# Performance work log

Hardware: AMD Instinct MI355X
Metric: run time of the kernel (lower is better)

The kernel has to match this reference:

```python
import jax, jax.numpy as jnp
import numpy as np

N = 50000      # nodes
F_IN = 512     # input features
HID = 128      # hidden
CLS = 64       # classes
E = 800000     # edges (avg degree 16)
EPS = 1e-5


def setup_inputs() -> dict:
    key = jax.random.key(0)
    k = jax.random.split(key, 6)
    x = jax.random.normal(k[0], (N, F_IN), jnp.float32)
    edge_index = jax.random.randint(k[1], (2, E), 0, N, dtype=jnp.int32)
    W1 = jax.random.normal(k[2], (F_IN, HID), jnp.float32) / np.float32(np.sqrt(F_IN))
    b1 = jnp.zeros((HID,), jnp.float32)
    W2 = jax.random.normal(k[3], (HID, CLS), jnp.float32) / np.float32(np.sqrt(HID))
    b2 = jnp.zeros((CLS,), jnp.float32)
    return {"x": x, "edge_index": edge_index, "W1": W1, "b1": b1, "W2": W2, "b2": b2}


def bin_active(x):
    # BinActive(scalar=True): per-node sign binarization scaled by mean |x| over features
    return jnp.sign(x) * jnp.mean(jnp.abs(x), axis=1, keepdims=True)


def bin_weight(w):
    # binarized weight with per-output-channel scaling (XNOR-style)
    return jnp.sign(w) * jnp.mean(jnp.abs(w), axis=0, keepdims=True)


def gcn_norm(edge_index, n):
    # add self-loops, symmetric D^-1/2 (A+I) D^-1/2 normalization (cached in original)
    loops = jnp.arange(n, dtype=edge_index.dtype)
    row = jnp.concatenate([edge_index[0], loops])  # source
    col = jnp.concatenate([edge_index[1], loops])  # target
    deg = jax.ops.segment_sum(jnp.ones(row.shape[0], jnp.float32), col, num_segments=n)
    dinv = jnp.where(deg > 0, jax.lax.rsqrt(jnp.maximum(deg, 1.0)), 0.0)
    return row, col, dinv[row] * dinv[col]


def bigcn_conv(x, W, b, row, col, norm, n):
    h = x @ bin_weight(W)                                   # [n, out]
    msg = norm[:, None] * h[row]                            # gather + scale, [E+n, out]
    return jax.ops.segment_sum(msg, col, num_segments=n) + b


def reference(x, edge_index, W1, b1, W2, b2):
    n = x.shape[0]
    # BatchNorm1d(affine=False), batch statistics (biased var)
    mu = jnp.mean(x, axis=0)
    var = jnp.var(x, axis=0)
    x = (x - mu) * jax.lax.rsqrt(var + EPS)
    row, col, norm = gcn_norm(edge_index, n)
    # layer loop: BinActive -> (dropout is identity in eval) -> BiGCNConv
    x = bigcn_conv(bin_active(x), W1, b1, row, col, norm, n)
    x = bigcn_conv(bin_active(x), W2, b2, row, col, norm, n)
    return jax.nn.log_softmax(x, axis=1)
```

## Files before the change

### kernel.cpp

```cpp
#include <hip/hip_runtime.h>

typedef unsigned long long u64;

#define F_IN 512
#define HID 128
#define CLS 64
#define EPS 1e-5f
#define NSB 512

__global__ __launch_bounds__(256) void col_stats_k(const float4* __restrict__ x4,
                                                   float* __restrict__ psum,
                                                   float* __restrict__ psq,
                                                   int n, int rpb) {
    __shared__ float red[256][9];
    int c4 = threadIdx.x & 127;
    int half = threadIdx.x >> 7;
    int r0 = blockIdx.x * rpb;
    int r1 = min(n, r0 + rpb);
    float s0=0.f,s1=0.f,s2=0.f,s3=0.f,q0=0.f,q1=0.f,q2=0.f,q3=0.f;
#pragma unroll 4
    for (int r = r0 + half; r < r1; r += 2) {
        float4 v = x4[(size_t)r * 128 + c4];
        s0 += v.x; q0 += v.x * v.x;
        s1 += v.y; q1 += v.y * v.y;
        s2 += v.z; q2 += v.z * v.z;
        s3 += v.w; q3 += v.w * v.w;
    }
    red[threadIdx.x][0]=s0; red[threadIdx.x][1]=s1; red[threadIdx.x][2]=s2; red[threadIdx.x][3]=s3;
    red[threadIdx.x][4]=q0; red[threadIdx.x][5]=q1; red[threadIdx.x][6]=q2; red[threadIdx.x][7]=q3;
    __syncthreads();
    if (half == 0) {
        int c = c4 * 4;
        float* os = &psum[(size_t)blockIdx.x * 512 + c];
        float* oq = &psq [(size_t)blockIdx.x * 512 + c];
        os[0] = s0 + red[c4+128][0]; os[1] = s1 + red[c4+128][1];
        os[2] = s2 + red[c4+128][2]; os[3] = s3 + red[c4+128][3];
        oq[0] = q0 + red[c4+128][4]; oq[1] = q1 + red[c4+128][5];
        oq[2] = q2 + red[c4+128][6]; oq[3] = q3 + red[c4+128][7];
    }
}

__global__ __launch_bounds__(256) void stats_reduce_k(const float* __restrict__ psum,
                                                      const float* __restrict__ psq,
                                                      float* __restrict__ mu,
                                                      float* __restrict__ rinv, int n) {
    __shared__ float reds[256], redq[256];
    int cc = threadIdx.x & 31;
    int bs = threadIdx.x >> 5;
    int c = blockIdx.x * 32 + cc;
    float s = 0.f, q = 0.f;
#pragma unroll 4
    for (int b = bs; b < NSB; b += 8) {
        s += psum[(size_t)b * 512 + c];
        q += psq [(size_t)b * 512 + c];
    }
    reds[threadIdx.x] = s; redq[threadIdx.x] = q;
    __syncthreads();
    if (bs == 0) {
#pragma unroll
        for (int t = 1; t < 8; ++t) { s += reds[cc + 32*t]; q += redq[cc + 32*t]; }
        float m = s / (float)n;
        float v = q / (float)n - m * m;
        mu[c] = m;
        rinv[c] = rsqrtf(v + EPS);
    }
}

__global__ __launch_bounds__(64) void pack_w1_k(const float* __restrict__ W,
                                                u64* __restrict__ sig,
                                                float* __restrict__ beta) {
    int j = blockIdx.x;
    int l = threadIdx.x;
    float asum = 0.f;
#pragma unroll
    for (int jw = 0; jw < 8; ++jw) {
        int f = (jw < 4) ? (4*l + jw) : (256 + 4*l + (jw - 4));
        float v = W[(size_t)f * HID + j];
        asum += fabsf(v);
        u64 b = __ballot(v > 0.0f);
        if (l == 0) sig[jw * HID + j] = b;
    }
    for (int m = 32; m >= 1; m >>= 1) asum += __shfl_xor(asum, m);
    if (l == 0) beta[j] = asum * (1.0f / 512.0f);
}

__global__ __launch_bounds__(64) void pack_w2_k(const float* __restrict__ W,
                                                float* __restrict__ sw4) {
    int j = blockIdx.x;
    int l = threadIdx.x;
    float v0 = W[(size_t)l * CLS + j];
    float v1 = W[(size_t)(l + 64) * CLS + j];
    float asum = fabsf(v0) + fabsf(v1);
    for (int m = 32; m >= 1; m >>= 1) asum += __shfl_xor(asum, m);
    float beta = asum * (1.0f / 128.0f);
    int f0 = l, f1 = l + 64;
    sw4[(f0 >> 2) * 256 + j * 4 + (f0 & 3)] = (v0 > 0.f) ? beta : -beta;
    sw4[(f1 >> 2) * 256 + j * 4 + (f1 & 3)] = (v1 > 0.f) ? beta : -beta;
}

__global__ __launch_bounds__(256) void deg_k(const int* __restrict__ col,
                                             int* __restrict__ deg, int e) {
    int i = blockIdx.x * blockDim.x + threadIdx.x;
    if (i < e) atomicAdd(&deg[col[i]], 1);
}

__global__ __launch_bounds__(256) void dinv_k(const int* __restrict__ deg,
                                              float* __restrict__ dinv, int n) {
    int i = blockIdx.x * blockDim.x + threadIdx.x;
    if (i < n) dinv[i] = rsqrtf((float)deg[i] + 1.0f);
}

__global__ __launch_bounds__(256) void scan_partial_k(const int* __restrict__ deg,
                                                      int* __restrict__ bsum, int n) {
    __shared__ int lds[256];
    int i = blockIdx.x * 256 + threadIdx.x;
    lds[threadIdx.x] = (i < n) ? deg[i] : 0;
    __syncthreads();
    for (int s = 128; s > 0; s >>= 1) {
        if (threadIdx.x < s) lds[threadIdx.x] += lds[threadIdx.x + s];
        __syncthreads();
    }
    if (threadIdx.x == 0) bsum[blockIdx.x] = lds[0];
}

__global__ __launch_bounds__(256) void scan_bsum_k(const int* __restrict__ bsum,
                                                   int* __restrict__ boff, int nb) {
    __shared__ int lds[256];
    int t = threadIdx.x;
    int v = (t < nb) ? bsum[t] : 0;
    lds[t] = v;
    __syncthreads();
    for (int s = 1; s < 256; s <<= 1) {
        int add = (t >= s) ? lds[t - s] : 0;
        __syncthreads();
        lds[t] += add;
        __syncthreads();
    }
    if (t < nb) boff[t] = lds[t] - v;
}

__global__ __launch_bounds__(256) void scan_final_k(const int* __restrict__ deg,
                                                    const int* __restrict__ boff,
                                                    int* __restrict__ offs,
                                                    int* __restrict__ cursor, int n) {
    __shared__ int lds[256];
    int t = threadIdx.x;
    int i = blockIdx.x * 256 + t;
    int v = (i < n) ? deg[i] : 0;
    lds[t] = v;
    __syncthreads();
    for (int s = 1; s < 256; s <<= 1) {
        int add = (t >= s) ? lds[t - s] : 0;
        __syncthreads();
        lds[t] += add;
        __syncthreads();
    }
    int excl = lds[t] - v + boff[blockIdx.x];
    if (i < n) { offs[i] = excl; cursor[i] = excl; }
}

__global__ __launch_bounds__(256) void fill_k(const int* __restrict__ row,
                                              const int* __restrict__ col,
                                              const float* __restrict__ dinv,
                                              int* __restrict__ cursor,
                                              int2* __restrict__ csr, int e) {
    int i = blockIdx.x * blockDim.x + threadIdx.x;
    if (i < e) {
        int r = row[i], c = col[i];
        int p = atomicAdd(&cursor[c], 1);
        float w = dinv[r] * dinv[c];
        csr[p] = make_int2(r, __float_as_int(w));
    }
}

__global__ __launch_bounds__(256) void bin1_gemm1_k(const float4* __restrict__ x4,
                                                    const float4* __restrict__ mu4,
                                                    const float4* __restrict__ rinv4,
                                                    const u64* __restrict__ sigW,
                                                    float* __restrict__ a1,
                                                    short2* __restrict__ dots, int n) {
    int tid = threadIdx.x;
    int wave = tid >> 6, l = tid & 63;
    int i = blockIdx.x * 4 + wave;
    if (i >= n) return;
    const float4* xr = x4 + (size_t)i * 128;
    float4 va = xr[l], vb = xr[64 + l];
    float4 ma = mu4[l], mb = mu4[64 + l];
    float4 ra = rinv4[l], rb = rinv4[64 + l];
    float t0 = va.x - ma.x, t1 = va.y - ma.y, t2 = va.z - ma.z, t3 = va.w - ma.w;
    float t4 = vb.x - mb.x, t5 = vb.y - mb.y, t6 = vb.z - mb.z, t7 = vb.w - mb.w;
    float asum = fabsf(t0)*ra.x + fabsf(t1)*ra.y + fabsf(t2)*ra.z + fabsf(t3)*ra.w
               + fabsf(t4)*rb.x + fabsf(t5)*rb.y + fabsf(t6)*rb.z + fabsf(t7)*rb.w;
    u64 sx[8];
    sx[0] = __ballot(t0 > 0.f); sx[1] = __ballot(t1 > 0.f);
    sx[2] = __ballot(t2 > 0.f); sx[3] = __ballot(t3 > 0.f);
    sx[4] = __ballot(t4 > 0.f); sx[5] = __ballot(t5 > 0.f);
    sx[6] = __ballot(t6 > 0.f); sx[7] = __ballot(t7 > 0.f);
    for (int m = 32; m >= 1; m >>= 1) asum += __shfl_xor(asum, m);
    if (l == 0) a1[i] = asum * (1.0f / 512.0f);
    int c0 = 0, c1 = 0;
#pragma unroll
    for (int w = 0; w < 8; ++w) {
        c0 += __popcll(sx[w] ^ sigW[w * HID + 2*l]);
        c1 += __popcll(sx[w] ^ sigW[w * HID + 2*l + 1]);
    }
    dots[(size_t)i * 64 + l] = make_short2((short)(512 - 2*c0), (short)(512 - 2*c1));
}

__global__ __launch_bounds__(256) void agg1_fused_k(const short2* __restrict__ dots,
                                                    const float* __restrict__ a1,
                                                    const int2* __restrict__ csr,
                                                    const int* __restrict__ offs,
                                                    const int* __restrict__ deg,
                                                    const float* __restrict__ dinv,
                                                    const float2* __restrict__ beta1_2,
                                                    const float2* __restrict__ b1_2,
                                                    u64* __restrict__ sig2x,
                                                    float* __restrict__ a2v, int n) {
    int tid = threadIdx.x;
    int wave = tid >> 6, l = tid & 63;
    int i = blockIdx.x * 4 + wave;
    if (i >= n) return;
    float di = dinv[i];
    float ts = di * di * a1[i];
    short2 ds = dots[(size_t)i * 64 + l];
    float acc0 = ts * (float)ds.x;
    float acc1 = ts * (float)ds.y;
    int off = offs[i], d = deg[i];
    int k = 0;
    for (; k + 4 <= d; k += 4) {
        int2 e0 = csr[off+k], e1 = csr[off+k+1], e2 = csr[off+k+2], e3 = csr[off+k+3];
        float t0 = __int_as_float(e0.y) * a1[e0.x];
        float t1 = __int_as_float(e1.y) * a1[e1.x];
        float t2 = __int_as_float(e2.y) * a1[e2.x];
        float t3 = __int_as_float(e3.y) * a1[e3.x];
        short2 d0 = dots[(size_t)e0.x * 64 + l];
        short2 d1 = dots[(size_t)e1.x * 64 + l];
        short2 d2 = dots[(size_t)e2.x * 64 + l];
        short2 d3 = dots[(size_t)e3.x * 64 + l];
        acc0 += t0*(float)d0.x + t1*(float)d1.x + t2*(float)d2.x + t3*(float)d3.x;
        acc1 += t0*(float)d0.y + t1*(float)d1.y + t2*(float)d2.y + t3*(float)d3.y;
    }
    for (; k < d; ++k) {
        int2 ew = csr[off + k];
        float t = __int_as_float(ew.y) * a1[ew.x];
        short2 dv = dots[(size_t)ew.x * 64 + l];
        acc0 += t * (float)dv.x;
        acc1 += t * (float)dv.y;
    }
    float2 be = beta1_2[l], bb = b1_2[l];
    acc0 = be.x * acc0 + bb.x;
    acc1 = be.y * acc1 + bb.y;
    float asum = fabsf(acc0) + fabsf(acc1);
    for (int m = 32; m >= 1; m >>= 1) asum += __shfl_xor(asum, m);
    u64 s0 = __ballot(acc0 > 0.f);
    u64 s1 = __ballot(acc1 > 0.f);
    if (l == 0) {
        sig2x[2 * (size_t)i]     = s0;
        sig2x[2 * (size_t)i + 1] = s1;
        a2v[i] = asum * (1.0f / 128.0f);
    }
}

__global__ __launch_bounds__(256) void aggz2_fused_k(const u64* __restrict__ sig2x,
                                                     const float* __restrict__ a2v,
                                                     const int2* __restrict__ csr,
                                                     const int* __restrict__ offs,
                                                     const int* __restrict__ deg,
                                                     const float* __restrict__ dinv,
                                                     const float* __restrict__ sw4,
                                                     const float* __restrict__ b2,
                                                     float* __restrict__ out, int n) {
    __shared__ float sw[CLS * HID];
    __shared__ float4 zbuf[4][32];
    int tid = threadIdx.x;
    for (int idx = tid; idx < CLS * HID; idx += 256) sw[idx] = sw4[idx];
    __syncthreads();
    int wave = tid >> 6, l = tid & 63;
    float bias = b2[l];
    for (int q = 0; q < 4; ++q) {
        int i = blockIdx.x * 16 + wave * 4 + q;
        if (i >= n) continue;
        float di = dinv[i];
        float ts = di * di * a2v[i];
        ulonglong2 ws = *(const ulonglong2*)&sig2x[2 * (size_t)i];
        float z0 = ((ws.x >> l) & 1) ? ts : -ts;
        float z1 = ((ws.y >> l) & 1) ? ts : -ts;
        int off = offs[i], d = deg[i];
        int k = 0;
        for (; k + 4 <= d; k += 4) {
            int2 e0 = csr[off+k], e1 = csr[off+k+1], e2 = csr[off+k+2], e3 = csr[off+k+3];
            ulonglong2 g0 = *(const ulonglong2*)&sig2x[2 * (size_t)e0.x];
            ulonglong2 g1 = *(const ulonglong2*)&sig2x[2 * (size_t)e1.x];
            ulonglong2 g2 = *(const ulonglong2*)&sig2x[2 * (size_t)e2.x];
            ulonglong2 g3 = *(const ulonglong2*)&sig2x[2 * (size_t)e3.x];
            float t0 = __int_as_float(e0.y) * a2v[e0.x];
            float t1 = __int_as_float(e1.y) * a2v[e1.x];
            float t2 = __int_as_float(e2.y) * a2v[e2.x];
            float t3 = __int_as_float(e3.y) * a2v[e3.x];
            z0 += (((g0.x>>l)&1) ? t0 : -t0) + (((g1.x>>l)&1) ? t1 : -t1)
                + (((g2.x>>l)&1) ? t2 : -t2) + (((g3.x>>l)&1) ? t3 : -t3);
            z1 += (((g0.y>>l)&1) ? t0 : -t0) + (((g1.y>>l)&1) ? t1 : -t1)
                + (((g2.y>>l)&1) ? t2 : -t2) + (((g3.y>>l)&1) ? t3 : -t3);
        }
        for (; k < d; ++k) {
            int2 ew = csr[off + k];
            ulonglong2 gs = *(const ulonglong2*)&sig2x[2 * (size_t)ew.x];
            float t = __int_as_float(ew.y) * a2v[ew.x];
            z0 += ((gs.x >> l) & 1) ? t : -t;
            z1 += ((gs.y >> l) & 1) ? t : -t;
        }
        ((float2*)&zbuf[wave][0])[l] = make_float2(z0, z1);
        float o = bias;
#pragma unroll
        for (int g = 0; g < 32; ++g) {
            float4 zz = zbuf[wave][g];
            float4 ww = *(const float4*)&sw[g * 256 + l * 4];
            o += zz.x*ww.x + zz.y*ww.y + zz.z*ww.z + zz.w*ww.w;
        }
        float m = o;
        for (int k2 = 32; k2 >= 1; k2 >>= 1) m = fmaxf(m, __shfl_xor(m, k2));
        float ev = __expf(o - m);
        float s = ev;
        for (int k2 = 32; k2 >= 1; k2 >>= 1) s += __shfl_xor(s, k2);
        out[(size_t)i * CLS + l] = o - m - __logf(s);
    }
}

extern "C" void kernel_launch(void* const* d_in, const int* in_sizes, int n_in,
                              void* d_out, int out_size, void* d_ws, size_t ws_size,
                              hipStream_t stream) {
    const float* x  = (const float*)d_in[0];
    const int*   ei = (const int*)d_in[1];
    const float* W1 = (const float*)d_in[2];
    const float* b1 = (const float*)d_in[3];
    const float* W2 = (const float*)d_in[4];
    const float* b2 = (const float*)d_in[5];
    float* out = (float*)d_out;

    const int n = in_sizes[0] / F_IN;
    const int e = in_sizes[1] / 2;
    const int* row = ei;
    const int* col = ei + e;

    char* w = (char*)d_ws;
    size_t off = 0;
    auto alloc = [&](size_t bytes) {
        void* p = w + off;
        off += (bytes + 255) & ~(size_t)255;
        return p;
    };
    int*   deg    = (int*)alloc((size_t)n * 4);
    size_t zero_bytes = off;
    float* psum   = (float*)alloc((size_t)NSB * 512 * 4);
    float* psq    = (float*)alloc((size_t)NSB * 512 * 4);
    float* mu     = (float*)alloc(F_IN * 4);
    float* rinv   = (float*)alloc(F_IN * 4);
    float* dinv   = (float*)alloc((size_t)n * 4);
    float* beta1  = (float*)alloc(HID * 4);
    u64*   sig1   = (u64*)alloc(HID * 8 * 8);
    float* sw4    = (float*)alloc(CLS * HID * 4);
    int*   offs   = (int*)alloc((size_t)n * 4);
    int*   cursor = (int*)alloc((size_t)n * 4);
    int*   bsum   = (int*)alloc(256 * 4);
    int*   boff   = (int*)alloc(256 * 4);
    int2*  csr    = (int2*)alloc((size_t)e * 8);
    short2* dots  = (short2*)alloc((size_t)n * 64 * 4);
    float* a1     = (float*)alloc((size_t)n * 4);
    u64*   sig2x  = (u64*)alloc((size_t)n * 2 * 8);
    float* a2v    = (float*)alloc((size_t)n * 4);
    (void)ws_size;

    hipMemsetAsync(d_ws, 0, zero_bytes, stream);

    int rpb = (n + NSB - 1) / NSB;
    col_stats_k<<<NSB, 256, 0, stream>>>((const float4*)x, psum, psq, n, rpb);
    stats_reduce_k<<<16, 256, 0, stream>>>(psum, psq, mu, rinv, n);
    pack_w1_k<<<HID, 64, 0, stream>>>(W1, sig1, beta1);
    pack_w2_k<<<CLS, 64, 0, stream>>>(W2, sw4);
    deg_k<<<(e + 255) / 256, 256, 0, stream>>>(col, deg, e);
    dinv_k<<<(n + 255) / 256, 256, 0, stream>>>(deg, dinv, n);

    int nb = (n + 255) / 256;
    scan_partial_k<<<nb, 256, 0, stream>>>(deg, bsum, n);
    scan_bsum_k<<<1, 256, 0, stream>>>(bsum, boff, nb);
    scan_final_k<<<nb, 256, 0, stream>>>(deg, boff, offs, cursor, n);
    fill_k<<<(e + 255) / 256, 256, 0, stream>>>(row, col, dinv, cursor, csr, e);

    bin1_gemm1_k<<<(n + 3) / 4, 256, 0, stream>>>((const float4*)x, (const float4*)mu,
                                                  (const float4*)rinv, sig1, a1, dots, n);
    agg1_fused_k<<<(n + 3) / 4, 256, 0, stream>>>(dots, a1, csr, offs, deg, dinv,
                                                  (const float2*)beta1, (const float2*)b1,
                                                  sig2x, a2v, n);
    aggz2_fused_k<<<(n + 15) / 16, 256, 0, stream>>>(sig2x, a2v, csr, offs, deg, dinv,
                                                     sw4, b2, out, n);
}
```

Before: 415.7 us.

## Pre-bake per-source scale factors into CSR edge weights for both aggregation layers

Fuses the dinv computation into the scan kernel and moves CSR fill after the first binarized GEMM, so each layer-1 edge weight already includes the source node's a1 scale. A second CSR copy is rescaled by a2v in a new rebake kernel before layer 2, which removes a random per-edge scale gather from both aggregation loops. Layer-2 aggregation now processes 16 nodes per wave instead of 4, amortizing the shared-memory load of W2, and that load plus the sig2x store are vectorized. In exchange it writes and reads an extra edge array and adds a full pass over the edges.

Result: slower. 435.1 us (+4.7%).

```diff
diff --git a/kernel.cpp b/kernel.cpp
--- a/kernel.cpp
+++ b/kernel.cpp
@@ -104,12 +104,6 @@
     if (i < e) atomicAdd(&deg[col[i]], 1);
 }
 
-__global__ __launch_bounds__(256) void dinv_k(const int* __restrict__ deg,
-                                              float* __restrict__ dinv, int n) {
-    int i = blockIdx.x * blockDim.x + threadIdx.x;
-    if (i < n) dinv[i] = rsqrtf((float)deg[i] + 1.0f);
-}
-
 __global__ __launch_bounds__(256) void scan_partial_k(const int* __restrict__ deg,
                                                       int* __restrict__ bsum, int n) {
     __shared__ int lds[256];
@@ -142,7 +136,8 @@
 __global__ __launch_bounds__(256) void scan_final_k(const int* __restrict__ deg,
                                                     const int* __restrict__ boff,
                                                     int* __restrict__ offs,
-                                                    int* __restrict__ cursor, int n) {
+                                                    int* __restrict__ cursor,
+                                                    float* __restrict__ dinv, int n) {
     __shared__ int lds[256];
     int t = threadIdx.x;
     int i = blockIdx.x * 256 + t;
@@ -156,20 +151,9 @@
         __syncthreads();
     }
     int excl = lds[t] - v + boff[blockIdx.x];
-    if (i < n) { offs[i] = excl; cursor[i] = excl; }
-}
-
-__global__ __launch_bounds__(256) void fill_k(const int* __restrict__ row,
-                                              const int* __restrict__ col,
-                                              const float* __restrict__ dinv,
-                                              int* __restrict__ cursor,
-                                              int2* __restrict__ csr, int e) {
-    int i = blockIdx.x * blockDim.x + threadIdx.x;
-    if (i < e) {
-        int r = row[i], c = col[i];
-        int p = atomicAdd(&cursor[c], 1);
-        float w = dinv[r] * dinv[c];
-        csr[p] = make_int2(r, __float_as_int(w));
+    if (i < n) {
+        offs[i] = excl; cursor[i] = excl;
+        dinv[i] = rsqrtf((float)v + 1.0f);
     }
 }
 
@@ -207,9 +191,26 @@
     dots[(size_t)i * 64 + l] = make_short2((short)(512 - 2*c0), (short)(512 - 2*c1));
 }
 
+__global__ __launch_bounds__(256) void fill_k(const int* __restrict__ row,
+                                              const int* __restrict__ col,
+                                              const float* __restrict__ dinv,
+                                              const float* __restrict__ a1,
+                                              int* __restrict__ cursor,
+                                              int2* __restrict__ csr1,
+                                              int2* __restrict__ csrw, int e) {
+    int i = blockIdx.x * blockDim.x + threadIdx.x;
+    if (i < e) {
+        int r = row[i], c = col[i];
+        int p = atomicAdd(&cursor[c], 1);
+        float w = dinv[r] * dinv[c];
+        csr1[p] = make_int2(r, __float_as_int(w * a1[r]));
+        csrw[p] = make_int2(r, __float_as_int(w));
+    }
+}
+
 __global__ __launch_bounds__(256) void agg1_fused_k(const short2* __restrict__ dots,
                                                     const float* __restrict__ a1,
-                                                    const int2* __restrict__ csr,
+                                                    const int2* __restrict__ csr1,
                                                     const int* __restrict__ offs,
                                                     const int* __restrict__ deg,
                                                     const float* __restrict__ dinv,
@@ -229,11 +230,11 @@
     int off = offs[i], d = deg[i];
     int k = 0;
     for (; k + 4 <= d; k += 4) {
-        int2 e0 = csr[off+k], e1 = csr[off+k+1], e2 = csr[off+k+2], e3 = csr[off+k+3];
-        float t0 = __int_as_float(e0.y) * a1[e0.x];
-        float t1 = __int_as_float(e1.y) * a1[e1.x];
-        float t2 = __int_as_float(e2.y) * a1[e2.x];
-        float t3 = __int_as_float(e3.y) * a1[e3.x];
+        int2 e0 = csr1[off+k], e1 = csr1[off+k+1], e2 = csr1[off+k+2], e3 = csr1[off+k+3];
+        float t0 = __int_as_float(e0.y);
+        float t1 = __int_as_float(e1.y);
+        float t2 = __int_as_float(e2.y);
+        float t3 = __int_as_float(e3.y);
         short2 d0 = dots[(size_t)e0.x * 64 + l];
         short2 d1 = dots[(size_t)e1.x * 64 + l];
         short2 d2 = dots[(size_t)e2.x * 64 + l];
@@ -242,8 +243,8 @@
         acc1 += t0*(float)d0.y + t1*(float)d1.y + t2*(float)d2.y + t3*(float)d3.y;
     }
     for (; k < d; ++k) {
-        int2 ew = csr[off + k];
-        float t = __int_as_float(ew.y) * a1[ew.x];
+        int2 ew = csr1[off + k];
+        float t = __int_as_float(ew.y);
         short2 dv = dots[(size_t)ew.x * 64 + l];
         acc0 += t * (float)dv.x;
         acc1 += t * (float)dv.y;
@@ -256,30 +257,40 @@
     u64 s0 = __ballot(acc0 > 0.f);
     u64 s1 = __ballot(acc1 > 0.f);
     if (l == 0) {
-        sig2x[2 * (size_t)i]     = s0;
-        sig2x[2 * (size_t)i + 1] = s1;
+        ulonglong2 pk; pk.x = s0; pk.y = s1;
+        *(ulonglong2*)&sig2x[2 * (size_t)i] = pk;
         a2v[i] = asum * (1.0f / 128.0f);
+    }
+}
+
+__global__ __launch_bounds__(256) void rebake_k(int2* __restrict__ csrw,
+                                                const float* __restrict__ a2v, int e) {
+    int i = blockIdx.x * blockDim.x + threadIdx.x;
+    if (i < e) {
+        int2 ew = csrw[i];
+        csrw[i] = make_int2(ew.x, __float_as_int(__int_as_float(ew.y) * a2v[ew.x]));
     }
 }
 
 __global__ __launch_bounds__(256) void aggz2_fused_k(const u64* __restrict__ sig2x,
                                                      const float* __restrict__ a2v,
-                                                     const int2* __restrict__ csr,
+                                                     const int2* __restrict__ csrw,
                                                      const int* __restrict__ offs,
                                                      const int* __restrict__ deg,
                                                      const float* __restrict__ dinv,
-                                                     const float* __restrict__ sw4,
+                                                     const float4* __restrict__ sw4,
                                                      const float* __restrict__ b2,
                                                      float* __restrict__ out, int n) {
     __shared__ float sw[CLS * HID];
-    __shared__ float4 zbuf[4][32];
+    __shared__ float zbuf[4][HID];
     int tid = threadIdx.x;
-    for (int idx = tid; idx < CLS * HID; idx += 256) sw[idx] = sw4[idx];
+    for (int idx = tid; idx < CLS * HID / 4; idx += 256)
+        *(float4*)&sw[idx * 4] = sw4[idx];
     __syncthreads();
     int wave = tid >> 6, l = tid & 63;
     float bias = b2[l];
-    for (int q = 0; q < 4; ++q) {
-        int i = blockIdx.x * 16 + wave * 4 + q;
+    for (int q = 0; q < 16; ++q) {
+        int i = blockIdx.x * 64 + wave * 16 + q;
         if (i >= n) continue;
         float di = dinv[i];
         float ts = di * di * a2v[i];
@@ -289,24 +300,24 @@
         int off = offs[i], d = deg[i];
         int k = 0;
         for (; k + 4 <= d; k += 4) {
-            int2 e0 = csr[off+k], e1 = csr[off+k+1], e2 = csr[off+k+2], e3 = csr[off+k+3];
+            int2 e0 = csrw[off+k], e1 = csrw[off+k+1], e2 = csrw[off+k+2], e3 = csrw[off+k+3];
             ulonglong2 g0 = *(const ulonglong2*)&sig2x[2 * (size_t)e0.x];
             ulonglong2 g1 = *(const ulonglong2*)&sig2x[2 * (size_t)e1.x];
             ulonglong2 g2 = *(const ulonglong2*)&sig2x[2 * (size_t)e2.x];
             ulonglong2 g3 = *(const ulonglong2*)&sig2x[2 * (size_t)e3.x];
-            float t0 = __int_as_float(e0.y) * a2v[e0.x];
-            float t1 = __int_as_float(e1.y) * a2v[e1.x];
-            float t2 = __int_as_float(e2.y) * a2v[e2.x];
-            float t3 = __int_as_float(e3.y) * a2v[e3.x];
+            float t0 = __int_as_float(e0.y);
+            float t1 = __int_as_float(e1.y);
+            float t2 = __int_as_float(e2.y);
+            float t3 = __int_as_float(e3.y);
             z0 += (((g0.x>>l)&1) ? t0 : -t0) + (((g1.x>>l)&1) ? t1 : -t1)
                 + (((g2.x>>l)&1) ? t2 : -t2) + (((g3.x>>l)&1) ? t3 : -t3);
             z1 += (((g0.y>>l)&1) ? t0 : -t0) + (((g1.y>>l)&1) ? t1 : -t1)
                 + (((g2.y>>l)&1) ? t2 : -t2) + (((g3.y>>l)&1) ? t3 : -t3);
         }
         for (; k < d; ++k) {
-            int2 ew = csr[off + k];
+            int2 ew = csrw[off + k];
             ulonglong2 gs = *(const ulonglong2*)&sig2x[2 * (size_t)ew.x];
-            float t = __int_as_float(ew.y) * a2v[ew.x];
+            float t = __int_as_float(ew.y);
             z0 += ((gs.x >> l) & 1) ? t : -t;
             z1 += ((gs.y >> l) & 1) ? t : -t;
         }
@@ -314,7 +325,7 @@
         float o = bias;
 #pragma unroll
         for (int g = 0; g < 32; ++g) {
-            float4 zz = zbuf[wave][g];
+            float4 zz = *(const float4*)&zbuf[wave][g * 4];
             float4 ww = *(const float4*)&sw[g * 256 + l * 4];
             o += zz.x*ww.x + zz.y*ww.y + zz.z*ww.z + zz.w*ww.w;
         }
@@ -364,7 +375,8 @@
     int*   cursor = (int*)alloc((size_t)n * 4);
     int*   bsum   = (int*)alloc(256 * 4);
     int*   boff   = (int*)alloc(256 * 4);
-    int2*  csr    = (int2*)alloc((size_t)e * 8);
+    int2*  csr1   = (int2*)alloc((size_t)e * 8);
+    int2*  csrw   = (int2*)alloc((size_t)e * 8);
     short2* dots  = (short2*)alloc((size_t)n * 64 * 4);
     float* a1     = (float*)alloc((size_t)n * 4);
     u64*   sig2x  = (u64*)alloc((size_t)n * 2 * 8);
@@ -379,19 +391,19 @@
     pack_w1_k<<<HID, 64, 0, stream>>>(W1, sig1, beta1);
     pack_w2_k<<<CLS, 64, 0, stream>>>(W2, sw4);
     deg_k<<<(e + 255) / 256, 256, 0, stream>>>(col, deg, e);
-    dinv_k<<<(n + 255) / 256, 256, 0, stream>>>(deg, dinv, n);
 
     int nb = (n + 255) / 256;
     scan_partial_k<<<nb, 256, 0, stream>>>(deg, bsum, n);
     scan_bsum_k<<<1, 256, 0, stream>>>(bsum, boff, nb);
-    scan_final_k<<<nb, 256, 0, stream>>>(deg, boff, offs, cursor, n);
-    fill_k<<<(e + 255) / 256, 256, 0, stream>>>(row, col, dinv, cursor, csr, e);
+    scan_final_k<<<nb, 256, 0, stream>>>(deg, boff, offs, cursor, dinv, n);
 
     bin1_gemm1_k<<<(n + 3) / 4, 256, 0, stream>>>((const float4*)x, (const float4*)mu,
                                                   (const float4*)rinv, sig1, a1, dots, n);
-    agg1_fused_k<<<(n + 3) / 4, 256, 0, stream>>>(dots, a1, csr, offs, deg, dinv,
+    fill_k<<<(e + 255) / 256, 256, 0, stream>>>(row, col, dinv, a1, cursor, csr1, csrw, e);
+    agg1_fused_k<<<(n + 3) / 4, 256, 0, stream>>>(dots, a1, csr1, offs, deg, dinv,
                                                   (const float2*)beta1, (const float2*)b1,
                                                   sig2x, a2v, n);
-    aggz2_fused_k<<<(n + 15) / 16, 256, 0, stream>>>(sig2x, a2v, csr, offs, deg, dinv,
-                                                     sw4, b2, out, n);
-}
+    rebake_k<<<(e + 255) / 256, 256, 0, stream>>>(csrw, a2v, e);
+    aggz2_fused_k<<<(n + 63) / 64, 256, 0, stream>>>(sig2x, a2v, csrw, offs, deg, dinv,
+                                                     (const float4*)sw4, b2, out, n);
+}
```

## Replace layer-2 aggregation and matmul with XNOR-popcount over binarized signatures

Applied to the files above, without the earlier changes.

Layer 2 is now computed per output class as the popcount of the XOR between each neighbour's 128-bit sign signature and the packed weight sign bits, scaled by the edge weight and the per-node scale. This removes the LDS-staged 128x64 float matmul and the per-lane z accumulation that came before it, and it exploits the fact that both operands are ±1 times a scale. The dinv computation is folded into scan_final, which drops one launch, and fill_k is moved after the layer-1 GEMM. The cost is that every lane now gathers the full signature for each edge, and the order of summation changes slightly.

Measured after the change: 384.9 us. -7.4%, faster.

```diff
diff --git a/kernel.cpp b/kernel.cpp
--- a/kernel.cpp
+++ b/kernel.cpp
@@ -85,29 +85,27 @@
 }
 
 __global__ __launch_bounds__(64) void pack_w2_k(const float* __restrict__ W,
-                                                float* __restrict__ sw4) {
+                                                ulonglong2* __restrict__ sigw2,
+                                                float* __restrict__ beta2) {
     int j = blockIdx.x;
     int l = threadIdx.x;
-    float v0 = W[(size_t)l * CLS + j];
-    float v1 = W[(size_t)(l + 64) * CLS + j];
+    float v0 = W[(size_t)(2 * l) * CLS + j];
+    float v1 = W[(size_t)(2 * l + 1) * CLS + j];
     float asum = fabsf(v0) + fabsf(v1);
+    u64 s0 = __ballot(v0 > 0.0f);
+    u64 s1 = __ballot(v1 > 0.0f);
     for (int m = 32; m >= 1; m >>= 1) asum += __shfl_xor(asum, m);
-    float beta = asum * (1.0f / 128.0f);
-    int f0 = l, f1 = l + 64;
-    sw4[(f0 >> 2) * 256 + j * 4 + (f0 & 3)] = (v0 > 0.f) ? beta : -beta;
-    sw4[(f1 >> 2) * 256 + j * 4 + (f1 & 3)] = (v1 > 0.f) ? beta : -beta;
+    if (l == 0) {
+        ulonglong2 t; t.x = s0; t.y = s1;
+        sigw2[j] = t;
+        beta2[j] = asum * (1.0f / 128.0f);
+    }
 }
 
 __global__ __launch_bounds__(256) void deg_k(const int* __restrict__ col,
                                              int* __restrict__ deg, int e) {
     int i = blockIdx.x * blockDim.x + threadIdx.x;
     if (i < e) atomicAdd(&deg[col[i]], 1);
-}
-
-__global__ __launch_bounds__(256) void dinv_k(const int* __restrict__ deg,
-                                              float* __restrict__ dinv, int n) {
-    int i = blockIdx.x * blockDim.x + threadIdx.x;
-    if (i < n) dinv[i] = rsqrtf((float)deg[i] + 1.0f);
 }
 
 __global__ __launch_bounds__(256) void scan_partial_k(const int* __restrict__ deg,
@@ -142,7 +140,8 @@
 __global__ __launch_bounds__(256) void scan_final_k(const int* __restrict__ deg,
                                                     const int* __restrict__ boff,
                                                     int* __restrict__ offs,
-                                                    int* __restrict__ cursor, int n) {
+                                                    int* __restrict__ cursor,
+                                                    float* __restrict__ dinv, int n) {
     __shared__ int lds[256];
     int t = threadIdx.x;
     int i = blockIdx.x * 256 + t;
@@ -156,7 +155,10 @@
         __syncthreads();
     }
     int excl = lds[t] - v + boff[blockIdx.x];
-    if (i < n) { offs[i] = excl; cursor[i] = excl; }
+    if (i < n) {
+        offs[i] = excl; cursor[i] = excl;
+        dinv[i] = rsqrtf((float)v + 1.0f);
+    }
 }
 
 __global__ __launch_bounds__(256) void fill_k(const int* __restrict__ row,
@@ -256,75 +258,66 @@
     u64 s0 = __ballot(acc0 > 0.f);
     u64 s1 = __ballot(acc1 > 0.f);
     if (l == 0) {
-        sig2x[2 * (size_t)i]     = s0;
-        sig2x[2 * (size_t)i + 1] = s1;
+        ulonglong2 pk; pk.x = s0; pk.y = s1;
+        *(ulonglong2*)&sig2x[2 * (size_t)i] = pk;
         a2v[i] = asum * (1.0f / 128.0f);
     }
 }
 
-__global__ __launch_bounds__(256) void aggz2_fused_k(const u64* __restrict__ sig2x,
-                                                     const float* __restrict__ a2v,
-                                                     const int2* __restrict__ csr,
-                                                     const int* __restrict__ offs,
-                                                     const int* __restrict__ deg,
-                                                     const float* __restrict__ dinv,
-                                                     const float* __restrict__ sw4,
-                                                     const float* __restrict__ b2,
-                                                     float* __restrict__ out, int n) {
-    __shared__ float sw[CLS * HID];
-    __shared__ float4 zbuf[4][32];
+__global__ __launch_bounds__(256) void agg2_pop_k(const u64* __restrict__ sig2x,
+                                                  const float* __restrict__ a2v,
+                                                  const int2* __restrict__ csr,
+                                                  const int* __restrict__ offs,
+                                                  const int* __restrict__ deg,
+                                                  const float* __restrict__ dinv,
+                                                  const ulonglong2* __restrict__ sigw2,
+                                                  const float* __restrict__ beta2,
+                                                  const float* __restrict__ b2,
+                                                  float* __restrict__ out, int n) {
     int tid = threadIdx.x;
-    for (int idx = tid; idx < CLS * HID; idx += 256) sw[idx] = sw4[idx];
-    __syncthreads();
     int wave = tid >> 6, l = tid & 63;
-    float bias = b2[l];
-    for (int q = 0; q < 4; ++q) {
-        int i = blockIdx.x * 16 + wave * 4 + q;
-        if (i >= n) continue;
-        float di = dinv[i];
-        float ts = di * di * a2v[i];
-        ulonglong2 ws = *(const ulonglong2*)&sig2x[2 * (size_t)i];
-        float z0 = ((ws.x >> l) & 1) ? ts : -ts;
-        float z1 = ((ws.y >> l) & 1) ? ts : -ts;
-        int off = offs[i], d = deg[i];
-        int k = 0;
-        for (; k + 4 <= d; k += 4) {
-            int2 e0 = csr[off+k], e1 = csr[off+k+1], e2 = csr[off+k+2], e3 = csr[off+k+3];
-            ulonglong2 g0 = *(const ulonglong2*)&sig2x[2 * (size_t)e0.x];
-            ulonglong2 g1 = *(const ulonglong2*)&sig2x[2 * (size_t)e1.x];
-            ulonglong2 g2 = *(const ulonglong2*)&sig2x[2 * (size_t)e2.x];
-            ulonglong2 g3 = *(const ulonglong2*)&sig2x[2 * (size_t)e3.x];
-            float t0 = __int_as_float(e0.y) * a2v[e0.x];
-            float t1 = __int_as_float(e1.y) * a2v[e1.x];
-            float t2 = __int_as_float(e2.y) * a2v[e2.x];
-            float t3 = __int_as_float(e3.y) * a2v[e3.x];
-            z0 += (((g0.x>>l)&1) ? t0 : -t0) + (((g1.x>>l)&1) ? t1 : -t1)
-                + (((g2.x>>l)&1) ? t2 : -t2) + (((g3.x>>l)&1) ? t3 : -t3);
-            z1 += (((g0.y>>l)&1) ? t0 : -t0) + (((g1.y>>l)&1) ? t1 : -t1)
-                + (((g2.y>>l)&1) ? t2 : -t2) + (((g3.y>>l)&1) ? t3 : -t3);
-        }
-        for (; k < d; ++k) {
-            int2 ew = csr[off + k];
-            ulonglong2 gs = *(const ulonglong2*)&sig2x[2 * (size_t)ew.x];
-            float t = __int_as_float(ew.y) * a2v[ew.x];
-            z0 += ((gs.x >> l) & 1) ? t : -t;
-            z1 += ((gs.y >> l) & 1) ? t : -t;
-        }
-        ((float2*)&zbuf[wave][0])[l] = make_float2(z0, z1);
-        float o = bias;
-#pragma unroll
-        for (int g = 0; g < 32; ++g) {
-            float4 zz = zbuf[wave][g];
-            float4 ww = *(const float4*)&sw[g * 256 + l * 4];
-            o += zz.x*ww.x + zz.y*ww.y + zz.z*ww.z + zz.w*ww.w;
-        }
-        float m = o;
-        for (int k2 = 32; k2 >= 1; k2 >>= 1) m = fmaxf(m, __shfl_xor(m, k2));
-        float ev = __expf(o - m);
-        float s = ev;
-        for (int k2 = 32; k2 >= 1; k2 >>= 1) s += __shfl_xor(s, k2);
-        out[(size_t)i * CLS + l] = o - m - __logf(s);
-    }
+    int i = blockIdx.x * 4 + wave;
+    if (i >= n) return;
+    ulonglong2 wsig = sigw2[l];
+    float bet = beta2[l], bias = b2[l];
+    float di = dinv[i];
+    float ts = di * di * a2v[i];
+    ulonglong2 ss = *(const ulonglong2*)&sig2x[2 * (size_t)i];
+    int dp = __popcll(ss.x ^ wsig.x) + __popcll(ss.y ^ wsig.y);
+    float acc = ts * (float)(128 - 2 * dp);
+    int off = offs[i], d = deg[i];
+    int k = 0;
+    for (; k + 4 <= d; k += 4) {
+        int2 e0 = csr[off+k], e1 = csr[off+k+1], e2 = csr[off+k+2], e3 = csr[off+k+3];
+        ulonglong2 g0 = *(const ulonglong2*)&sig2x[2 * (size_t)e0.x];
+        ulonglong2 g1 = *(const ulonglong2*)&sig2x[2 * (size_t)e1.x];
+        ulonglong2 g2 = *(const ulonglong2*)&sig2x[2 * (size_t)e2.x];
+        ulonglong2 g3 = *(const ulonglong2*)&sig2x[2 * (size_t)e3.x];
+        float t0 = __int_as_float(e0.y) * a2v[e0.x];
+        float t1 = __int_as_float(e1.y) * a2v[e1.x];
+        float t2 = __int_as_float(e2.y) * a2v[e2.x];
+        float t3 = __int_as_float(e3.y) * a2v[e3.x];
+        int p0 = __popcll(g0.x ^ wsig.x) + __popcll(g0.y ^ wsig.y);
+        int p1 = __popcll(g1.x ^ wsig.x) + __popcll(g1.y ^ wsig.y);
+        int p2 = __popcll(g2.x ^ wsig.x) + __popcll(g2.y ^ wsig.y);
+        int p3 = __popcll(g3.x ^ wsig.x) + __popcll(g3.y ^ wsig.y);
+        acc += t0 * (float)(128 - 2*p0) + t1 * (float)(128 - 2*p1)
+             + t2 * (float)(128 - 2*p2) + t3 * (float)(128 - 2*p3);
+    }
+    for (; k < d; ++k) {
+        int2 ew = csr[off + k];
+        ulonglong2 gs = *(const ulonglong2*)&sig2x[2 * (size_t)ew.x];
+        float t = __int_as_float(ew.y) * a2v[ew.x];
+        int p = __popcll(gs.x ^ wsig.x) + __popcll(gs.y ^ wsig.y);
+        acc += t * (float)(128 - 2*p);
+    }
+    float o = bet * acc + bias;
+    float m = o;
+    for (int k2 = 32; k2 >= 1; k2 >>= 1) m = fmaxf(m, __shfl_xor(m, k2));
+    float ev = __expf(o - m);
+    float s = ev;
+    for (int k2 = 32; k2 >= 1; k2 >>= 1) s += __shfl_xor(s, k2);
+    out[(size_t)i * CLS + l] = o - m - __logf(s);
 }
 
 extern "C" void kernel_launch(void* const* d_in, const int* in_sizes, int n_in,
@@ -359,7 +352,8 @@
     float* dinv   = (float*)alloc((size_t)n * 4);
     float* beta1  = (float*)alloc(HID * 4);
     u64*   sig1   = (u64*)alloc(HID * 8 * 8);
-    float* sw4    = (float*)alloc(CLS * HID * 4);
+    ulonglong2* sigw2 = (ulonglong2*)alloc(CLS * 16);
+    float* beta2  = (float*)alloc(CLS * 4);
     int*   offs   = (int*)alloc((size_t)n * 4);
     int*   cursor = (int*)alloc((size_t)n * 4);
     int*   bsum   = (int*)alloc(256 * 4);
@@ -377,21 +371,20 @@
     col_stats_k<<<NSB, 256, 0, stream>>>((const float4*)x, psum, psq, n, rpb);
     stats_reduce_k<<<16, 256, 0, stream>>>(psum, psq, mu, rinv, n);
     pack_w1_k<<<HID, 64, 0, stream>>>(W1, sig1, beta1);
-    pack_w2_k<<<CLS, 64, 0, stream>>>(W2, sw4);
+    pack_w2_k<<<CLS, 64, 0, stream>>>(W2, sigw2, beta2);
     deg_k<<<(e + 255) / 256, 256, 0, stream>>>(col, deg, e);
-    dinv_k<<<(n + 255) / 256, 256, 0, stream>>>(deg, dinv, n);
 
     int nb = (n + 255) / 256;
     scan_partial_k<<<nb, 256, 0, stream>>>(deg, bsum, n);
     scan_bsum_k<<<1, 256, 0, stream>>>(bsum, boff, nb);
-    scan_final_k<<<nb, 256, 0, stream>>>(deg, boff, offs, cursor, n);
-    fill_k<<<(e + 255) / 256, 256, 0, stream>>>(row, col, dinv, cursor, csr, e);
+    scan_final_k<<<nb, 256, 0, stream>>>(deg, boff, offs, cursor, dinv, n);
 
     bin1_gemm1_k<<<(n + 3) / 4, 256, 0, stream>>>((const float4*)x, (const float4*)mu,
                                                   (const float4*)rinv, sig1, a1, dots, n);
+    fill_k<<<(e + 255) / 256, 256, 0, stream>>>(row, col, dinv, cursor, csr, e);
     agg1_fused_k<<<(n + 3) / 4, 256, 0, stream>>>(dots, a1, csr, offs, deg, dinv,
                                                   (const float2*)beta1, (const float2*)b1,
                                                   sig2x, a2v, n);
-    aggz2_fused_k<<<(n + 15) / 16, 256, 0, stream>>>(sig2x, a2v, csr, offs, deg, dinv,
-                                                     sw4, b2, out, n);
-}
+    agg2_pop_k<<<(n + 3) / 4, 256, 0, stream>>>(sig2x, a2v, csr, offs, deg, dinv,
+                                                sigw2, beta2, b2, out, n);
+}
```
